# Kernel tuning notes

Measured on AMD Instinct MI355X. Metric: run time of the kernel, lower is better.

The kernel has to match this reference:

```python
import jax, jax.numpy as jnp
import numpy as np

BINS = jnp.array([1, 2, 3, 4, 8, 16, 32, 64], dtype=jnp.int32)
L = 10      # max span width
HID = 150   # Score hidden dim


def _mlp(x, W1, b1, W2, b2, W3, b3):
    # Score module: Linear -> ReLU -> Linear -> ReLU -> Linear (dropout = identity at eval)
    h = jax.nn.relu(x @ W1 + b1)
    h = jax.nn.relu(h @ W2 + b2)
    return h @ W3 + b3


def setup_inputs() -> dict:
    key = jax.random.key(0)
    ks = jax.random.split(key, 16)
    T, A, E, D, S = 8192, 1024, 512, 20, 32768
    GI = 2 * A + E + D  # 2580
    sc = lambda n: 1.0 / np.sqrt(n)
    return {
        "states": jax.random.normal(ks[0], (T, A), jnp.float32),
        "embeds": jax.random.normal(ks[1], (T, E), jnp.float32),
        "span_starts": jnp.sort(jax.random.randint(ks[2], (S,), 0, T - L)),
        "span_lengths": jax.random.randint(ks[3], (S,), 0, L),
        # attention Score params (attn_dim -> 150 -> 150 -> 1)
        "Wa1": jax.random.normal(ks[4], (A, HID), jnp.float32) * sc(A),
        "ba1": jnp.zeros((HID,), jnp.float32),
        "Wa2": jax.random.normal(ks[5], (HID, HID), jnp.float32) * sc(HID),
        "ba2": jnp.zeros((HID,), jnp.float32),
        "Wa3": jax.random.normal(ks[6], (HID, 1), jnp.float32) * sc(HID),
        "ba3": jnp.zeros((1,), jnp.float32),
        # Distance embedding table (len(bins)+1 = 9 buckets)
        "width_table": jax.random.normal(ks[7], (9, D), jnp.float32) * 0.1,
        # mention Score params (gi_dim -> 150 -> 150 -> 1)
        "Ws1": jax.random.normal(ks[8], (GI, HID), jnp.float32) * sc(GI),
        "bs1": jnp.zeros((HID,), jnp.float32),
        "Ws2": jax.random.normal(ks[9], (HID, HID), jnp.float32) * sc(HID),
        "bs2": jnp.zeros((HID,), jnp.float32),
        "Ws3": jax.random.normal(ks[10], (HID, 1), jnp.float32) * sc(HID),
        "bs3": jnp.zeros((1,), jnp.float32),
    }


def reference(states, embeds, span_starts, span_lengths,
              Wa1, ba1, Wa2, ba2, Wa3, ba3,
              width_table,
              Ws1, bs1, Ws2, bs2, Ws3, bs3):
    T = states.shape[0]
    # per-token attention logits: [T, 1]
    attns = _mlp(states, Wa1, ba1, Wa2, ba2, Wa3, ba3)

    pos = jnp.arange(L)
    idx = span_starts[:, None] + pos[None, :]                 # [S, L]
    mask = pos[None, :] <= span_lengths[:, None]              # valid positions
    idx = jnp.minimum(idx, T - 1)

    span_attn = jnp.where(mask, attns[idx, 0], -jnp.inf)      # [S, L]
    w = jax.nn.softmax(span_attn, axis=1)                     # per-span softmax
    pooled = jnp.einsum('sl,sle->se', w, embeds[idx])         # [S, E]

    ends = span_starts + span_lengths
    widths = span_lengths + 1
    bucket = jnp.searchsorted(BINS, widths.astype(jnp.int32), side='right')
    size_emb = width_table[bucket]                            # [S, D]

    g = jnp.concatenate([states[span_starts], states[ends], pooled, size_emb], axis=-1)
    scores = _mlp(g, Ws1, bs1, Ws2, bs2, Ws3, bs3)[:, 0]      # [S]
    return scores
```

## Files before the change

### kernel.cpp

```cpp
#include <hip/hip_runtime.h>
#include <math.h>

#define T_TOK 8192
#define A_DIM 1024
#define E_DIM 512
#define S_SPAN 32768
#define HID 150

typedef __attribute__((ext_vector_type(8))) short short8;
typedef __attribute__((ext_vector_type(4))) float f32x4;
typedef __attribute__((ext_vector_type(4))) unsigned int u32x4;

__device__ __forceinline__ unsigned short f2bf(float f) {
    unsigned int u = __builtin_bit_cast(unsigned int, f);
    u += 0x7FFFu + ((u >> 16) & 1u);
    return (unsigned short)(u >> 16);
}
__device__ __forceinline__ float bf2f(unsigned int h16) {
    unsigned int u = h16 << 16;
    return __builtin_bit_cast(float, u);
}
__device__ __forceinline__ short8 cast8(f32x4 a, f32x4 b) {
    short8 r;
    r[0] = (short)f2bf(a.x); r[1] = (short)f2bf(a.y);
    r[2] = (short)f2bf(a.z); r[3] = (short)f2bf(a.w);
    r[4] = (short)f2bf(b.x); r[5] = (short)f2bf(b.y);
    r[6] = (short)f2bf(b.z); r[7] = (short)f2bf(b.w);
    return r;
}

struct WConv { const float* src; unsigned short* dst; int K0; int Kpad; int nblk; };
struct PrepTab {
    WConv g[6];
    const float* wt; const float* Ws1w; float* PW;
};

__global__ __launch_bounds__(256) void prep_kernel(PrepTab tab) {
    int b = blockIdx.x;
    #pragma unroll
    for (int gi = 0; gi < 6; ++gi) {
        if (b < tab.g[gi].nblk) {
            int idx = b * 256 + threadIdx.x;
            int Kpad = tab.g[gi].Kpad;
            if (idx < Kpad * 160) {
                int k = idx / 160, j = idx - k * 160;
                float v = (j < HID && k < tab.g[gi].K0)
                          ? tab.g[gi].src[(size_t)k * HID + j] : 0.f;
                tab.g[gi].dst[(size_t)j * Kpad + k] = f2bf(v);
            }
            return;
        }
        b -= tab.g[gi].nblk;
    }
    int j = threadIdx.x;
    if (j < HID) {
        float acc = 0.f;
        for (int k = 0; k < 20; ++k)
            acc = fmaf(tab.wt[b * 20 + k], tab.Ws1w[k * HID + j], acc);
        tab.PW[b * HID + j] = acc;
    }
}

struct GG {
    const void* A; int lda;
    const unsigned short* W; int K; int nrb;
    unsigned short* outh; int ldo;
    const float* bias; int relu;
    const float* dotv; const float* dotb; float* dotout;
    const unsigned short* W2; const float* bias2;
};
struct GTab { GG g[4]; int ng; };

template <int TAG, bool AF32>
__global__ __launch_bounds__(256) void gemm_fused(GTab tab) {
    constexpr int LDW = 72;
    __shared__ unsigned short WtL[2][160 * LDW];

    int b = blockIdx.x;
    int gi = 0;
    while (gi < tab.ng - 1 && b >= tab.g[gi].nrb) { b -= tab.g[gi].nrb; ++gi; }
    const GG G = tab.g[gi];

    const int tid = threadIdx.x;
    const int wid = tid >> 6;
    const int lane = tid & 63;
    const int l15 = lane & 15;
    const int quad = lane >> 4;
    const int row0 = b * 64 + wid * 16 + l15;
    const int K = G.K;
    const int nch = K >> 6;
    const float* Af = (const float*)G.A + (size_t)row0 * G.lda;
    const unsigned short* Ah = (const unsigned short*)G.A + (size_t)row0 * G.lda;

    u32x4 stg[5];
    int sn[5], sk[5];
    #pragma unroll
    for (int i = 0; i < 5; ++i) { int u = tid + i * 256; sn[i] = u >> 3; sk[i] = (u & 7) * 8; }

    f32x4 acc[10];
    #pragma unroll
    for (int nt = 0; nt < 10; ++nt) acc[nt] = (f32x4){0.f, 0.f, 0.f, 0.f};

    #pragma unroll
    for (int i = 0; i < 5; ++i)
        stg[i] = *(const u32x4*)(G.W + (size_t)sn[i] * K + sk[i]);
    short8 avc0, avc1;
    if (AF32) {
        f32x4 f0 = *(const f32x4*)(Af + quad * 8);
        f32x4 f1 = *(const f32x4*)(Af + quad * 8 + 4);
        f32x4 f2 = *(const f32x4*)(Af + 32 + quad * 8);
        f32x4 f3 = *(const f32x4*)(Af + 32 + quad * 8 + 4);
        avc0 = cast8(f0, f1);
        avc1 = cast8(f2, f3);
    } else {
        avc0 = *(const short8*)(Ah + quad * 8);
        avc1 = *(const short8*)(Ah + 32 + quad * 8);
    }
    #pragma unroll
    for (int i = 0; i < 5; ++i)
        *(u32x4*)&WtL[0][sn[i] * LDW + sk[i]] = stg[i];
    __syncthreads();

    for (int c = 0; c < nch; ++c) {
        const int pb = c & 1;
        short8 avn0, avn1;
        f32x4 fn0, fn1, fn2, fn3;
        const bool more = (c + 1 < nch);
        if (more) {
            const int kn = (c + 1) << 6;
            #pragma unroll
            for (int i = 0; i < 5; ++i)
                stg[i] = *(const u32x4*)(G.W + (size_t)sn[i] * K + kn + sk[i]);
            if (AF32) {
                fn0 = *(const f32x4*)(Af + kn + quad * 8);
                fn1 = *(const f32x4*)(Af + kn + quad * 8 + 4);
                fn2 = *(const f32x4*)(Af + kn + 32 + quad * 8);
                fn3 = *(const f32x4*)(Af + kn + 32 + quad * 8 + 4);
            } else {
                avn0 = *(const short8*)(Ah + kn + quad * 8);
                avn1 = *(const short8*)(Ah + kn + 32 + quad * 8);
            }
        }
        #pragma unroll
        for (int nt = 0; nt < 10; ++nt) {
            short8 bv0 = *(const short8*)&WtL[pb][(nt * 16 + l15) * LDW + quad * 8];
            acc[nt] = __builtin_amdgcn_mfma_f32_16x16x32_bf16(avc0, bv0, acc[nt], 0, 0, 0);
            short8 bv1 = *(const short8*)&WtL[pb][(nt * 16 + l15) * LDW + 32 + quad * 8];
            acc[nt] = __builtin_amdgcn_mfma_f32_16x16x32_bf16(avc1, bv1, acc[nt], 0, 0, 0);
        }
        if (more) {
            #pragma unroll
            for (int i = 0; i < 5; ++i)
                *(u32x4*)&WtL[pb ^ 1][sn[i] * LDW + sk[i]] = stg[i];
            if (AF32) {
                avc0 = cast8(fn0, fn1);
                avc1 = cast8(fn2, fn3);
            } else {
                avc0 = avn0; avc1 = avn1;
            }
        }
        __syncthreads();
    }

    const int rbase = b * 64 + wid * 16 + quad * 4;
    if (G.W2) {
        constexpr int LDH = 168;
        unsigned short* tile = &WtL[0][0] + wid * 16 * LDH;
        #pragma unroll
        for (int nt = 0; nt < 10; ++nt) {
            int col = nt * 16 + l15;
            float bv_ = (col < HID) ? G.bias[col] : 0.f;
            #pragma unroll
            for (int r = 0; r < 4; ++r) {
                float v = fmaxf(acc[nt][r] + bv_, 0.f);
                tile[(quad * 4 + r) * LDH + col] = f2bf(v);
            }
        }
        f32x4 acc2[10];
        #pragma unroll
        for (int nt = 0; nt < 10; ++nt) acc2[nt] = (f32x4){0.f, 0.f, 0.f, 0.f};
        #pragma unroll
        for (int kc = 0; kc < 5; ++kc) {
            short8 av = *(const short8*)&tile[l15 * LDH + kc * 32 + quad * 8];
            #pragma unroll
            for (int nt = 0; nt < 10; ++nt) {
                short8 bv = *(const short8*)(G.W2 + (size_t)(nt * 16 + l15) * 192 + kc * 32 + quad * 8);
                acc2[nt] = __builtin_amdgcn_mfma_f32_16x16x32_bf16(av, bv, acc2[nt], 0, 0, 0);
            }
        }
        float part[4] = {0.f, 0.f, 0.f, 0.f};
        #pragma unroll
        for (int nt = 0; nt < 10; ++nt) {
            int col = nt * 16 + l15;
            float b2 = (col < HID) ? G.bias2[col] : 0.f;
            float vv = (col < HID) ? G.dotv[col] : 0.f;
            #pragma unroll
            for (int r = 0; r < 4; ++r)
                part[r] += fmaxf(acc2[nt][r] + b2, 0.f) * vv;
        }
        #pragma unroll
        for (int r = 0; r < 4; ++r) {
            float p = part[r];
            #pragma unroll
            for (int off = 1; off < 16; off <<= 1) p += __shfl_xor(p, off);
            if (l15 == 0) G.dotout[rbase + r] = p + G.dotb[0];
        }
    } else if (G.dotout) {
        float part[4] = {0.f, 0.f, 0.f, 0.f};
        #pragma unroll
        for (int nt = 0; nt < 10; ++nt) {
            int col = nt * 16 + l15;
            float bv_ = (col < HID) ? G.bias[col] : 0.f;
            float vv = (col < HID) ? G.dotv[col] : 0.f;
            #pragma unroll
            for (int r = 0; r < 4; ++r)
                part[r] += fmaxf(acc[nt][r] + bv_, 0.f) * vv;
        }
        #pragma unroll
        for (int r = 0; r < 4; ++r) {
            float p = part[r];
            #pragma unroll
            for (int off = 1; off < 16; off <<= 1) p += __shfl_xor(p, off);
            if (l15 == 0) G.dotout[rbase + r] = p + G.dotb[0];
        }
    } else {
        #pragma unroll
        for (int nt = 0; nt < 10; ++nt) {
            int col = nt * 16 + l15;
            float bv_ = (G.bias != nullptr && col < HID) ? G.bias[col] : 0.f;
            #pragma unroll
            for (int r = 0; r < 4; ++r) {
                int row = rbase + r;
                float v = acc[nt][r] + bv_;
                if (G.relu) v = fmaxf(v, 0.f);
                G.outh[(size_t)row * G.ldo + col] = f2bf(v);
            }
        }
    }
}

__global__ __launch_bounds__(256) void span_l1_kernel(const float* __restrict__ attns,
                                                      const int* __restrict__ starts,
                                                      const int* __restrict__ lens,
                                                      const unsigned short* __restrict__ Ps,
                                                      const unsigned short* __restrict__ Pe,
                                                      const unsigned short* __restrict__ Pm,
                                                      const float* __restrict__ PW,
                                                      const float* __restrict__ bs1,
                                                      unsigned short* __restrict__ SH1) {
    const int wid = threadIdx.x >> 6;
    const int lane = threadIdx.x & 63;
    const int grp = lane >> 4;
    const int hl = lane & 15;
    const int gbase = lane & 48;
    const int s = blockIdx.x * 16 + wid * 4 + grp;
    const int start = starts[s];
    const int len = lens[s];

    const int iv = min(start + hl, T_TOK - 1);
    float a = (hl <= len) ? attns[iv] : -INFINITY;
    float m = a;
    #pragma unroll
    for (int off = 8; off; off >>= 1) m = fmaxf(m, __shfl_xor(m, off));
    float e = (hl <= len) ? __expf(a - m) : 0.f;
    float ssum = e;
    #pragma unroll
    for (int off = 8; off; off >>= 1) ssum += __shfl_xor(ssum, off);
    float wv = e / ssum;

    float wl[10]; int il[10];
    #pragma unroll
    for (int l = 0; l < 10; ++l) {
        wl[l] = __shfl(wv, gbase + l);
        il[l] = __shfl(iv, gbase + l);
    }

    const int end = start + len;
    const int width = len + 1;
    const int bucket = (width >= 1) + (width >= 2) + (width >= 3) + (width >= 4) +
                       (width >= 8) + (width >= 16) + (width >= 32) + (width >= 64);

    const unsigned short* ps = Ps + (size_t)start * 160;
    const unsigned short* pe = Pe + (size_t)end * 160;
    const float* pw = PW + bucket * HID;

    for (int p = hl; p < 75; p += 16) {
        const int j = 2 * p;
        unsigned int u0 = *(const unsigned int*)(ps + j);
        unsigned int u1 = *(const unsigned int*)(pe + j);
        float a0 = bs1[j]     + bf2f(u0 & 0xffff) + bf2f(u1 & 0xffff) + pw[j];
        float a1 = bs1[j + 1] + bf2f(u0 >> 16)    + bf2f(u1 >> 16)    + pw[j + 1];
        #pragma unroll
        for (int l = 0; l < 10; ++l) {
            unsigned int um = *(const unsigned int*)(Pm + (size_t)il[l] * 160 + j);
            a0 = fmaf(wl[l], bf2f(um & 0xffff), a0);
            a1 = fmaf(wl[l], bf2f(um >> 16), a1);
        }
        unsigned int packed = (unsigned int)f2bf(fmaxf(a0, 0.f)) |
                              ((unsigned int)f2bf(fmaxf(a1, 0.f)) << 16);
        *(unsigned int*)(SH1 + (size_t)s * 192 + j) = packed;
    }
}

extern "C" void kernel_launch(void* const* d_in, const int* in_sizes, int n_in,
                              void* d_out, int out_size, void* d_ws, size_t ws_size,
                              hipStream_t stream) {
    const float* states = (const float*)d_in[0];
    const float* embeds = (const float*)d_in[1];
    const int* span_starts = (const int*)d_in[2];
    const int* span_lengths = (const int*)d_in[3];
    const float* Wa1 = (const float*)d_in[4];
    const float* ba1 = (const float*)d_in[5];
    const float* Wa2 = (const float*)d_in[6];
    const float* ba2 = (const float*)d_in[7];
    const float* Wa3 = (const float*)d_in[8];
    const float* ba3 = (const float*)d_in[9];
    const float* width_table = (const float*)d_in[10];
    const float* Ws1 = (const float*)d_in[11];
    const float* bs1 = (const float*)d_in[12];
    const float* Ws2 = (const float*)d_in[13];
    const float* bs2 = (const float*)d_in[14];
    const float* Ws3 = (const float*)d_in[15];
    const float* bs3 = (const float*)d_in[16];
    float* out = (float*)d_out;

    char* w = (char*)d_ws;
    unsigned short* WtA  = (unsigned short*)w;  w += 480 * 1024 * 2;
    unsigned short* WtE  = (unsigned short*)w;  w += 160 * 512 * 2;
    unsigned short* Wa2t = (unsigned short*)w;  w += 160 * 192 * 2;
    unsigned short* Ws2t = (unsigned short*)w;  w += 160 * 192 * 2;
    float* PW    = (float*)w;                   w += 5632;
    float* attns = (float*)w;                   w += 8192 * 4;
    unsigned short* Psh = (unsigned short*)w;   w += (size_t)T_TOK * 160 * 2;
    unsigned short* Peh = (unsigned short*)w;   w += (size_t)T_TOK * 160 * 2;
    unsigned short* Pmh = (unsigned short*)w;   w += (size_t)T_TOK * 160 * 2;
    unsigned short* SH1 = (unsigned short*)w;   w += (size_t)S_SPAN * 192 * 2;

    PrepTab pt;
    pt.g[0] = { Wa1,              WtA,              1024, 1024, (160*1024 + 255)/256 };
    pt.g[1] = { Ws1,              WtA + 160*1024,   1024, 1024, (160*1024 + 255)/256 };
    pt.g[2] = { Ws1 + 1024*150,   WtA + 320*1024,   1024, 1024, (160*1024 + 255)/256 };
    pt.g[3] = { Ws1 + 2048*150,   WtE,               512,  512, (160*512  + 255)/256 };
    pt.g[4] = { Wa2,              Wa2t,              150,  192, (160*192  + 255)/256 };
    pt.g[5] = { Ws2,              Ws2t,              150,  192, (160*192  + 255)/256 };
    pt.wt = width_table; pt.Ws1w = Ws1 + 2560*150; pt.PW = PW;
    int wblk = 0; for (int i = 0; i < 6; ++i) wblk += pt.g[i].nblk;
    prep_kernel<<<wblk + 9, 256, 0, stream>>>(pt);

    GG z = {};

    GTab t1; t1.ng = 4;
    t1.g[0] = z; t1.g[0].A = states; t1.g[0].lda = 1024; t1.g[0].W = WtA;            t1.g[0].K = 1024;
    t1.g[0].nrb = 128; t1.g[0].bias = ba1;
    t1.g[0].W2 = Wa2t; t1.g[0].bias2 = ba2;
    t1.g[0].dotv = Wa3; t1.g[0].dotb = ba3; t1.g[0].dotout = attns;
    t1.g[1] = z; t1.g[1].A = states; t1.g[1].lda = 1024; t1.g[1].W = WtA + 160*1024; t1.g[1].K = 1024;
    t1.g[1].nrb = 128; t1.g[1].outh = Psh; t1.g[1].ldo = 160;
    t1.g[2] = z; t1.g[2].A = states; t1.g[2].lda = 1024; t1.g[2].W = WtA + 320*1024; t1.g[2].K = 1024;
    t1.g[2].nrb = 128; t1.g[2].outh = Peh; t1.g[2].ldo = 160;
    t1.g[3] = z; t1.g[3].A = embeds; t1.g[3].lda = 512;  t1.g[3].W = WtE;            t1.g[3].K = 512;
    t1.g[3].nrb = 128; t1.g[3].outh = Pmh; t1.g[3].ldo = 160;
    gemm_fused<1, true><<<512, 256, 0, stream>>>(t1);

    span_l1_kernel<<<S_SPAN / 16, 256, 0, stream>>>(attns, span_starts, span_lengths,
                                                    Psh, Peh, Pmh, PW, bs1, SH1);

    GTab t3; t3.ng = 1;
    t3.g[0] = z; t3.g[0].A = SH1; t3.g[0].lda = 192; t3.g[0].W = Ws2t; t3.g[0].K = 192;
    t3.g[0].nrb = 512; t3.g[0].bias = bs2; t3.g[0].dotv = Ws3; t3.g[0].dotb = bs3; t3.g[0].dotout = out;
    gemm_fused<3, false><<<512, 256, 0, stream>>>(t3);
}
```

Measured before the change: 165.8 us.

## Fuse span layer-1 gather with layer-2 MFMA and score dot into one kernel

Merges the span gather/softmax/layer-1 kernel with the following layer-2 GEMM and final dot product. The layer-1 activations stay in per-wave shared-memory tiles instead of going through the global SH1 buffer. Each lane now owns one span and does the softmax serially, loading 8 bf16 values per access. The bias is folded into the width table during prep. This removes one launch and the global write and re-read of the hidden activations. In exchange, layer-2 weights are read straight from global memory by every wave, and the kernel uses more registers.

```diff
diff --git a/kernel.cpp b/kernel.cpp
--- a/kernel.cpp
+++ b/kernel.cpp
@@ -32,7 +32,7 @@
 struct WConv { const float* src; unsigned short* dst; int K0; int Kpad; int nblk; };
 struct PrepTab {
     WConv g[6];
-    const float* wt; const float* Ws1w; float* PW;
+    const float* wt; const float* Ws1w; const float* bs1; float* PW;
 };
 
 __global__ __launch_bounds__(256) void prep_kernel(PrepTab tab) {
@@ -53,11 +53,14 @@
         b -= tab.g[gi].nblk;
     }
     int j = threadIdx.x;
-    if (j < HID) {
+    if (j < 160) {
         float acc = 0.f;
-        for (int k = 0; k < 20; ++k)
-            acc = fmaf(tab.wt[b * 20 + k], tab.Ws1w[k * HID + j], acc);
-        tab.PW[b * HID + j] = acc;
+        if (j < HID) {
+            for (int k = 0; k < 20; ++k)
+                acc = fmaf(tab.wt[b * 20 + k], tab.Ws1w[k * HID + j], acc);
+            acc += tab.bs1[j];
+        }
+        tab.PW[b * 160 + j] = acc;
     }
 }
 
@@ -239,66 +242,117 @@
     }
 }
 
-__global__ __launch_bounds__(256) void span_l1_kernel(const float* __restrict__ attns,
-                                                      const int* __restrict__ starts,
-                                                      const int* __restrict__ lens,
-                                                      const unsigned short* __restrict__ Ps,
-                                                      const unsigned short* __restrict__ Pe,
-                                                      const unsigned short* __restrict__ Pm,
-                                                      const float* __restrict__ PW,
-                                                      const float* __restrict__ bs1,
-                                                      unsigned short* __restrict__ SH1) {
+__device__ __forceinline__ void add_bf8(f32x4& A, f32x4& B, u32x4 u) {
+    A.x += bf2f(u.x & 0xffff); A.y += bf2f(u.x >> 16);
+    A.z += bf2f(u.y & 0xffff); A.w += bf2f(u.y >> 16);
+    B.x += bf2f(u.z & 0xffff); B.y += bf2f(u.z >> 16);
+    B.z += bf2f(u.w & 0xffff); B.w += bf2f(u.w >> 16);
+}
+__device__ __forceinline__ void fma_bf8(f32x4& A, f32x4& B, u32x4 u, float w) {
+    A.x = fmaf(w, bf2f(u.x & 0xffff), A.x); A.y = fmaf(w, bf2f(u.x >> 16), A.y);
+    A.z = fmaf(w, bf2f(u.y & 0xffff), A.z); A.w = fmaf(w, bf2f(u.y >> 16), A.w);
+    B.x = fmaf(w, bf2f(u.z & 0xffff), B.x); B.y = fmaf(w, bf2f(u.z >> 16), B.y);
+    B.z = fmaf(w, bf2f(u.w & 0xffff), B.z); B.w = fmaf(w, bf2f(u.w >> 16), B.w);
+}
+
+__global__ __launch_bounds__(256) void span_fused_kernel(
+        const float* __restrict__ attns,
+        const int* __restrict__ starts,
+        const int* __restrict__ lens,
+        const unsigned short* __restrict__ Ps,
+        const unsigned short* __restrict__ Pe,
+        const unsigned short* __restrict__ Pm,
+        const float* __restrict__ PW,
+        const unsigned short* __restrict__ W2,
+        const float* __restrict__ bs2,
+        const float* __restrict__ Ws3,
+        const float* __restrict__ bs3,
+        float* __restrict__ out) {
+    constexpr int LDH = 200;
+    __shared__ unsigned short tileAll[4][16 * LDH];
     const int wid = threadIdx.x >> 6;
     const int lane = threadIdx.x & 63;
-    const int grp = lane >> 4;
-    const int hl = lane & 15;
-    const int gbase = lane & 48;
-    const int s = blockIdx.x * 16 + wid * 4 + grp;
+    const int r = lane & 15;
+    const int q = lane >> 4;
+    unsigned short* tile = &tileAll[wid][0];
+    const int s = blockIdx.x * 64 + wid * 16 + r;
+
     const int start = starts[s];
     const int len = lens[s];
-
-    const int iv = min(start + hl, T_TOK - 1);
-    float a = (hl <= len) ? attns[iv] : -INFINITY;
-    float m = a;
-    #pragma unroll
-    for (int off = 8; off; off >>= 1) m = fmaxf(m, __shfl_xor(m, off));
-    float e = (hl <= len) ? __expf(a - m) : 0.f;
-    float ssum = e;
-    #pragma unroll
-    for (int off = 8; off; off >>= 1) ssum += __shfl_xor(ssum, off);
-    float wv = e / ssum;
-
-    float wl[10]; int il[10];
-    #pragma unroll
-    for (int l = 0; l < 10; ++l) {
-        wl[l] = __shfl(wv, gbase + l);
-        il[l] = __shfl(iv, gbase + l);
-    }
-
     const int end = start + len;
     const int width = len + 1;
     const int bucket = (width >= 1) + (width >= 2) + (width >= 3) + (width >= 4) +
                        (width >= 8) + (width >= 16) + (width >= 32) + (width >= 64);
 
+    int il[10];
+    float wgt[10];
+    float m = -INFINITY;
+    #pragma unroll
+    for (int l = 0; l < 10; ++l) {
+        int iv = min(start + l, T_TOK - 1);
+        il[l] = iv * 160;
+        wgt[l] = (l <= len) ? attns[iv] : -INFINITY;
+        m = fmaxf(m, wgt[l]);
+    }
+    float ssum = 0.f;
+    #pragma unroll
+    for (int l = 0; l < 10; ++l) { wgt[l] = __expf(wgt[l] - m); ssum += wgt[l]; }
+    const float inv = 1.f / ssum;
+    #pragma unroll
+    for (int l = 0; l < 10; ++l) wgt[l] *= inv;
+
     const unsigned short* ps = Ps + (size_t)start * 160;
     const unsigned short* pe = Pe + (size_t)end * 160;
-    const float* pw = PW + bucket * HID;
-
-    for (int p = hl; p < 75; p += 16) {
-        const int j = 2 * p;
-        unsigned int u0 = *(const unsigned int*)(ps + j);
-        unsigned int u1 = *(const unsigned int*)(pe + j);
-        float a0 = bs1[j]     + bf2f(u0 & 0xffff) + bf2f(u1 & 0xffff) + pw[j];
-        float a1 = bs1[j + 1] + bf2f(u0 >> 16)    + bf2f(u1 >> 16)    + pw[j + 1];
-        #pragma unroll
-        for (int l = 0; l < 10; ++l) {
-            unsigned int um = *(const unsigned int*)(Pm + (size_t)il[l] * 160 + j);
-            a0 = fmaf(wl[l], bf2f(um & 0xffff), a0);
-            a1 = fmaf(wl[l], bf2f(um >> 16), a1);
-        }
-        unsigned int packed = (unsigned int)f2bf(fmaxf(a0, 0.f)) |
-                              ((unsigned int)f2bf(fmaxf(a1, 0.f)) << 16);
-        *(unsigned int*)(SH1 + (size_t)s * 192 + j) = packed;
+    const float* pw = PW + bucket * 160;
+
+    #pragma unroll
+    for (int i = 0; i < 5; ++i) {
+        const int j0 = (q + 4 * i) * 8;
+        f32x4 a0 = *(const f32x4*)(pw + j0);
+        f32x4 a1 = *(const f32x4*)(pw + j0 + 4);
+        add_bf8(a0, a1, *(const u32x4*)(ps + j0));
+        add_bf8(a0, a1, *(const u32x4*)(pe + j0));
+        #pragma unroll
+        for (int l = 0; l < 10; ++l)
+            fma_bf8(a0, a1, *(const u32x4*)(Pm + il[l] + j0), wgt[l]);
+        u32x4 pk;
+        pk.x = (unsigned)f2bf(fmaxf(a0.x, 0.f)) | ((unsigned)f2bf(fmaxf(a0.y, 0.f)) << 16);
+        pk.y = (unsigned)f2bf(fmaxf(a0.z, 0.f)) | ((unsigned)f2bf(fmaxf(a0.w, 0.f)) << 16);
+        pk.z = (unsigned)f2bf(fmaxf(a1.x, 0.f)) | ((unsigned)f2bf(fmaxf(a1.y, 0.f)) << 16);
+        pk.w = (unsigned)f2bf(fmaxf(a1.z, 0.f)) | ((unsigned)f2bf(fmaxf(a1.w, 0.f)) << 16);
+        *(u32x4*)&tile[r * LDH + j0] = pk;
+    }
+
+    f32x4 acc[10];
+    #pragma unroll
+    for (int nt = 0; nt < 10; ++nt) acc[nt] = (f32x4){0.f, 0.f, 0.f, 0.f};
+    #pragma unroll
+    for (int kc = 0; kc < 5; ++kc) {
+        short8 av = *(const short8*)&tile[r * LDH + kc * 32 + q * 8];
+        #pragma unroll
+        for (int nt = 0; nt < 10; ++nt) {
+            short8 bv = *(const short8*)(W2 + (size_t)(nt * 16 + r) * 192 + kc * 32 + q * 8);
+            acc[nt] = __builtin_amdgcn_mfma_f32_16x16x32_bf16(av, bv, acc[nt], 0, 0, 0);
+        }
+    }
+
+    float part[4] = {0.f, 0.f, 0.f, 0.f};
+    #pragma unroll
+    for (int nt = 0; nt < 10; ++nt) {
+        int col = nt * 16 + r;
+        float b2 = (col < HID) ? bs2[col] : 0.f;
+        float vv = (col < HID) ? Ws3[col] : 0.f;
+        #pragma unroll
+        for (int rr = 0; rr < 4; ++rr)
+            part[rr] += fmaxf(acc[nt][rr] + b2, 0.f) * vv;
+    }
+    const int rbase = blockIdx.x * 64 + wid * 16 + q * 4;
+    #pragma unroll
+    for (int rr = 0; rr < 4; ++rr) {
+        float p = part[rr];
+        #pragma unroll
+        for (int off = 1; off < 16; off <<= 1) p += __shfl_xor(p, off);
+        if (r == 0) out[rbase + rr] = p + bs3[0];
     }
 }
 
@@ -329,12 +383,11 @@
     unsigned short* WtE  = (unsigned short*)w;  w += 160 * 512 * 2;
     unsigned short* Wa2t = (unsigned short*)w;  w += 160 * 192 * 2;
     unsigned short* Ws2t = (unsigned short*)w;  w += 160 * 192 * 2;
-    float* PW    = (float*)w;                   w += 5632;
+    float* PW    = (float*)w;                   w += 9 * 160 * 4;
     float* attns = (float*)w;                   w += 8192 * 4;
     unsigned short* Psh = (unsigned short*)w;   w += (size_t)T_TOK * 160 * 2;
     unsigned short* Peh = (unsigned short*)w;   w += (size_t)T_TOK * 160 * 2;
     unsigned short* Pmh = (unsigned short*)w;   w += (size_t)T_TOK * 160 * 2;
-    unsigned short* SH1 = (unsigned short*)w;   w += (size_t)S_SPAN * 192 * 2;
 
     PrepTab pt;
     pt.g[0] = { Wa1,              WtA,              1024, 1024, (160*1024 + 255)/256 };
@@ -343,7 +396,7 @@
     pt.g[3] = { Ws1 + 2048*150,   WtE,               512,  512, (160*512  + 255)/256 };
     pt.g[4] = { Wa2,              Wa2t,              150,  192, (160*192  + 255)/256 };
     pt.g[5] = { Ws2,              Ws2t,              150,  192, (160*192  + 255)/256 };
-    pt.wt = width_table; pt.Ws1w = Ws1 + 2560*150; pt.PW = PW;
+    pt.wt = width_table; pt.Ws1w = Ws1 + 2560*150; pt.bs1 = bs1; pt.PW = PW;
     int wblk = 0; for (int i = 0; i < 6; ++i) wblk += pt.g[i].nblk;
     prep_kernel<<<wblk + 9, 256, 0, stream>>>(pt);
 
@@ -362,11 +415,7 @@
     t1.g[3].nrb = 128; t1.g[3].outh = Pmh; t1.g[3].ldo = 160;
     gemm_fused<1, true><<<512, 256, 0, stream>>>(t1);
 
-    span_l1_kernel<<<S_SPAN / 16, 256, 0, stream>>>(attns, span_starts, span_lengths,
-                                                    Psh, Peh, Pmh, PW, bs1, SH1);
-
-    GTab t3; t3.ng = 1;
-    t3.g[0] = z; t3.g[0].A = SH1; t3.g[0].lda = 192; t3.g[0].W = Ws2t; t3.g[0].K = 192;
-    t3.g[0].nrb = 512; t3.g[0].bias = bs2; t3.g[0].dotv = Ws3; t3.g[0].dotb = bs3; t3.g[0].dotout = out;
-    gemm_fused<3, false><<<512, 256, 0, stream>>>(t3);
-}
+    span_fused_kernel<<<S_SPAN / 64, 256, 0, stream>>>(attns, span_starts, span_lengths,
+                                                       Psh, Peh, Pmh, PW, Ws2t,
+                                                       bs2, Ws3, bs3, out);
+}
```

New measurement: 172.4 us. 4.0% more time.
